# Performance work log

Measured on AMD Instinct MI355X. Metric: run time of the kernel, lower is better.

Reference implementation:

```python
import jax, jax.numpy as jnp
import numpy as np

D_MODEL = 768
NHEAD = 12
DK = D_MODEL // NHEAD
MAX_DIST = 1000.0
FF = 3072
POS_HIDDEN = 32  # hidden width of the relative-position bias MLP
EPS = 1e-5
B, L = 2, 1024


def setup_inputs() -> dict:
    key = jax.random.key(0)
    ks = jax.random.split(key, 24)

    def lin(k, i, o):  # torch-Linear-like init, stored as (in, out)
        return jax.random.uniform(k, (i, o), jnp.float32, -1.0, 1.0) / np.sqrt(i)

    return {
        "src": jax.random.normal(ks[0], (B, L, D_MODEL), jnp.float32),
        "src_x": jax.random.uniform(ks[1], (B, L), jnp.float32) * 1000.0,
        "src_y": jax.random.uniform(ks[2], (B, L), jnp.float32) * 1000.0,
        # attention projections (q,k,v,out)
        "Wq": lin(ks[3], D_MODEL, D_MODEL), "bq": jnp.zeros((D_MODEL,), jnp.float32),
        "Wk": lin(ks[4], D_MODEL, D_MODEL), "bk": jnp.zeros((D_MODEL,), jnp.float32),
        "Wv": lin(ks[5], D_MODEL, D_MODEL), "bv": jnp.zeros((D_MODEL,), jnp.float32),
        "Wo": lin(ks[6], D_MODEL, D_MODEL), "bo": jnp.zeros((D_MODEL,), jnp.float32),
        # relative-position bias MLP: 2 -> POS_HIDDEN -> NHEAD
        "P1": lin(ks[7], 2, POS_HIDDEN), "pb1": jnp.zeros((POS_HIDDEN,), jnp.float32),
        "P2": lin(ks[8], POS_HIDDEN, NHEAD), "pb2": jnp.zeros((NHEAD,), jnp.float32),
        # FFN
        "W1": lin(ks[9], D_MODEL, FF), "b1": jnp.zeros((FF,), jnp.float32),
        "W2": lin(ks[10], FF, D_MODEL), "b2": jnp.zeros((D_MODEL,), jnp.float32),
        # post-LN params
        "g1": jnp.ones((D_MODEL,), jnp.float32), "be1": jnp.zeros((D_MODEL,), jnp.float32),
        "g2": jnp.ones((D_MODEL,), jnp.float32), "be2": jnp.zeros((D_MODEL,), jnp.float32),
    }


def _layernorm(x, g, b):
    m = jnp.mean(x, axis=-1, keepdims=True)
    v = jnp.var(x, axis=-1, keepdims=True)
    return (x - m) * jax.lax.rsqrt(v + EPS) * g + b


def reference(src, src_x, src_y, Wq, bq, Wk, bk, Wv, bv, Wo, bo,
              P1, pb1, P2, pb2, W1, b1, W2, b2, g1, be1, g2, be2):
    b, l, _ = src.shape
    # projections -> (b, h, l, dk)
    q = (src @ Wq + bq).reshape(b, l, NHEAD, DK).transpose(0, 2, 1, 3)
    k = (src @ Wk + bk).reshape(b, l, NHEAD, DK).transpose(0, 2, 1, 3)
    v = (src @ Wv + bv).reshape(b, l, NHEAD, DK).transpose(0, 2, 1, 3)
    # 2D relative positions, clipped and normalized to [-1, 1]
    rx = jnp.clip(src_x[:, :, None] - src_x[:, None, :], -MAX_DIST, MAX_DIST) / MAX_DIST
    ry = jnp.clip(src_y[:, :, None] - src_y[:, None, :], -MAX_DIST, MAX_DIST) / MAX_DIST
    rel = jnp.stack([rx, ry], axis=-1)                        # (b, l, l, 2)
    bias = jax.nn.relu(rel @ P1 + pb1) @ P2 + pb2             # (b, l, l, h)
    bias = bias.transpose(0, 3, 1, 2)                         # (b, h, l, l)
    scores = jnp.einsum('bhqd,bhkd->bhqk', q, k) / np.sqrt(DK).astype(np.float32) + bias
    attn = jax.nn.softmax(scores, axis=-1)
    o = jnp.einsum('bhqk,bhkd->bhqd', attn, v).transpose(0, 2, 1, 3).reshape(b, l, D_MODEL)
    src2 = o @ Wo + bo
    x = _layernorm(src + src2, g1, be1)                       # post-LN residual 1
    ff = jax.nn.relu(x @ W1 + b1) @ W2 + b2                   # FFN
    return _layernorm(x + ff, g2, be2)                        # post-LN residual 2
```

## Files before the change

### kernel.cpp

```cpp
#include <hip/hip_runtime.h>
#include <math.h>

typedef unsigned short ushort_t;
typedef __attribute__((ext_vector_type(8))) short bf16x8;
typedef __attribute__((ext_vector_type(4))) float f32x4;

constexpr int kD      = 768;
constexpr int kNH     = 12;
constexpr int kDK     = 64;
constexpr int kFF     = 3072;
constexpr int kL      = 1024;
constexpr int kRows   = 2048;
constexpr float kEPS  = 1e-5f;

__device__ __forceinline__ ushort_t f2bf(float f) {
    union { float f; unsigned u; } v; v.f = f;
    unsigned r = (v.u + 0x7fffu + ((v.u >> 16) & 1u)) >> 16;
    return (ushort_t)r;
}
__device__ __forceinline__ float bf2f(ushort_t u) {
    union { unsigned u; float f; } v; v.u = ((unsigned)u) << 16; return v.f;
}

#define GL_LDS(gp, lp) __builtin_amdgcn_global_load_lds( \
    (const __attribute__((address_space(1))) void*)(gp), \
    (__attribute__((address_space(3))) void*)(lp), 16, 0, 0)

template<int RELU, int OUTBF, int ADDBIAS>
__device__ __forceinline__ void gemm_body(const ushort_t* __restrict__ A,
                                          const ushort_t* __restrict__ WT,
                                          const float* __restrict__ bias,
                                          void* __restrict__ Cout,
                                          int N, int K, int row0, int col0,
                                          int kbeg, int kend, ushort_t* lds)
{
    ushort_t* As = lds;
    ushort_t* Bs = lds + 4096;

    const int tid  = threadIdx.x;
    const int lane = tid & 63;
    const int wave = tid >> 6;
    const int wrow = (wave & 1) * 64;
    const int wcol = (wave >> 1) * 64;

    const int srow = wave * 16 + (lane >> 2);
    const int sk   = (lane & 3) * 8;
    const ushort_t* ga0 = A  + (size_t)(row0 + srow)      * K + sk;
    const ushort_t* ga1 = A  + (size_t)(row0 + srow + 64) * K + sk;
    const ushort_t* gb0 = WT + (size_t)(col0 + srow)      * K + sk;
    const ushort_t* gb1 = WT + (size_t)(col0 + srow + 64) * K + sk;
    ushort_t* la0 = As + wave * 512;
    ushort_t* la1 = As + 2048 + wave * 512;
    ushort_t* lb0 = Bs + wave * 512;
    ushort_t* lb1 = Bs + 2048 + wave * 512;

    const int fl = lane & 15, fq = lane >> 4;
    const ushort_t* fa[4];
    const ushort_t* fb[4];
    #pragma unroll
    for (int i = 0; i < 4; ++i) {
        fa[i] = As + (wrow + i * 16 + fl) * 32 + fq * 8;
        fb[i] = Bs + (wcol + i * 16 + fl) * 32 + fq * 8;
    }

    f32x4 acc[4][4] = {};

    for (int k0 = kbeg; k0 < kend; k0 += 32) {
        __syncthreads();
        GL_LDS(ga0 + k0, la0);
        GL_LDS(ga1 + k0, la1);
        GL_LDS(gb0 + k0, lb0);
        GL_LDS(gb1 + k0, lb1);
        __syncthreads();

        bf16x8 av[4], bv[4];
        #pragma unroll
        for (int i = 0; i < 4; ++i) {
            av[i] = *(const bf16x8*)fa[i];
            bv[i] = *(const bf16x8*)fb[i];
        }
        #pragma unroll
        for (int mi = 0; mi < 4; ++mi)
            #pragma unroll
            for (int ni = 0; ni < 4; ++ni)
                acc[mi][ni] = __builtin_amdgcn_mfma_f32_16x16x32_bf16(
                    av[mi], bv[ni], acc[mi][ni], 0, 0, 0);
    }

    #pragma unroll
    for (int mi = 0; mi < 4; ++mi) {
        const int m = wrow + mi * 16 + fq * 4;
        #pragma unroll
        for (int ni = 0; ni < 4; ++ni) {
            const int n = wcol + ni * 16 + fl;
            const float bb = ADDBIAS ? bias[col0 + n] : 0.f;
            #pragma unroll
            for (int r = 0; r < 4; ++r) {
                float v = acc[mi][ni][r] + bb;
                if (RELU) v = fmaxf(v, 0.f);
                const size_t idx = (size_t)(row0 + m + r) * N + col0 + n;
                if (OUTBF) ((ushort_t*)Cout)[idx] = f2bf(v);
                else       ((float*)Cout)[idx]    = v;
            }
        }
    }
}

template<int RELU, int OUTBF>
__global__ __launch_bounds__(256)
void gemm_kernel(const ushort_t* __restrict__ A, const ushort_t* __restrict__ WT,
                 const float* __restrict__ bias, void* __restrict__ Cout,
                 int N, int K)
{
    __shared__ ushort_t lds[8192];
    gemm_body<RELU, OUTBF, 1>(A, WT, bias, Cout, N, K,
                              blockIdx.y * 128, blockIdx.x * 128, 0, K, lds);
}

__global__ __launch_bounds__(256)
void gemm_splitk_kernel(const ushort_t* __restrict__ A, const ushort_t* __restrict__ WT,
                        float* __restrict__ parts, int N, int K, int kslice)
{
    __shared__ ushort_t lds[8192];
    const int z = blockIdx.z;
    float* out = parts + (size_t)z * kRows * N;
    gemm_body<0, 0, 0>(A, WT, nullptr, out, N, K,
                       blockIdx.y * 128, blockIdx.x * 128,
                       z * kslice, (z + 1) * kslice, lds);
}

__device__ __forceinline__ void wt_tile(const float* __restrict__ src,
                                        ushort_t* __restrict__ dst,
                                        int K, int N, int kt, int nt,
                                        float (*T)[65], int tid)
{
    #pragma unroll
    for (int i = 0; i < 4; ++i) {
        const int e = tid + i * 256;
        const int r = e >> 4;
        const int c = (e & 15) * 4;
        const float4 f = *(const float4*)&src[(size_t)(kt + r) * N + nt + c];
        T[c + 0][r] = f.x; T[c + 1][r] = f.y; T[c + 2][r] = f.z; T[c + 3][r] = f.w;
    }
    __syncthreads();
    #pragma unroll
    for (int i = 0; i < 4; ++i) {
        const int e = tid + i * 256;
        const int n = e >> 4;
        const int kc = (e & 15) * 4;
        ushort4 o;
        o.x = f2bf(T[n][kc + 0]); o.y = f2bf(T[n][kc + 1]);
        o.z = f2bf(T[n][kc + 2]); o.w = f2bf(T[n][kc + 3]);
        *(ushort4*)&dst[(size_t)(nt + n) * K + kt + kc] = o;
    }
}

__global__ __launch_bounds__(256)
void prep_kernel(const float* __restrict__ Wq, const float* __restrict__ Wk,
                 const float* __restrict__ Wv,
                 ushort_t* wqT, ushort_t* wkT, ushort_t* wvT,
                 const float* __restrict__ src, ushort_t* __restrict__ sb)
{
    __shared__ float T[64][65];
    const int bid = blockIdx.x;
    const int tid = threadIdx.x;

    if (bid < 432) {
        const int wz = bid / 144, t = bid - wz * 144;
        const float* s = (wz == 0) ? Wq : (wz == 1) ? Wk : Wv;
        ushort_t*   d = (wz == 0) ? wqT : (wz == 1) ? wkT : wvT;
        wt_tile(s, d, kD, kD, (t % 12) * 64, (t / 12) * 64, T, tid);
    } else {
        const int i = (bid - 432) * 256 + tid;
        const float4 f = ((const float4*)src)[i];
        ushort4 o;
        o.x = f2bf(f.x); o.y = f2bf(f.y); o.z = f2bf(f.z); o.w = f2bf(f.w);
        ((ushort4*)sb)[i] = o;
    }
}

struct BiasSmem {
    float P[32][16];
    float pb2l[12];
    float qxl[16], qyl[16], kxl[64], kyl[64];
    ushort_t Btile[12 * 1024];
};
struct AttnSmem {
    ushort_t Sp[4][16][72];
    ushort_t Ob[4][16][64];
    float    Ll[4][16];
};

__device__ __forceinline__ void bias_body(int bid, BiasSmem& S,
                 const float* __restrict__ sx, const float* __restrict__ sy,
                 const float* __restrict__ P1, const float* __restrict__ pb1,
                 const float* __restrict__ P2, const float* __restrict__ pb2,
                 ushort_t* __restrict__ biasb)
{
    const int b  = bid >> 10;
    const int qt = (bid >> 4) & 63;
    const int kt = bid & 15;
    const int tid = threadIdx.x;

    if (tid < 32) {
        S.P[tid][0] = P1[tid];
        S.P[tid][1] = P1[32 + tid];
        S.P[tid][2] = pb1[tid];
        S.P[tid][3] = 0.f;
    }
    for (int e = tid; e < 384; e += 256) S.P[e / 12][4 + e % 12] = P2[e];
    if (tid < 12) S.pb2l[tid] = pb2[tid];
    if (tid < 16) { S.qxl[tid] = sx[b * kL + qt * 16 + tid];
                    S.qyl[tid] = sy[b * kL + qt * 16 + tid]; }
    if (tid < 64) { S.kxl[tid] = sx[b * kL + kt * 64 + tid];
                    S.kyl[tid] = sy[b * kL + kt * 64 + tid]; }
    __syncthreads();

    const int ri = tid >> 4;
    const int fl = tid & 15;
    const int fq = ri >> 2, r = ri & 3;
    const int lane16 = fq * 16 + fl;
    const float xi = S.qxl[ri], yi = S.qyl[ri];

    float rx[4], ry[4];
    #pragma unroll
    for (int n = 0; n < 4; ++n) {
        const int cj = n * 16 + fl;
        rx[n] = fminf(fmaxf(xi - S.kxl[cj], -1000.f), 1000.f) * 1e-3f;
        ry[n] = fminf(fmaxf(yi - S.kyl[cj], -1000.f), 1000.f) * 1e-3f;
    }

    float acc[4][12] = {};
    #pragma unroll 4
    for (int u = 0; u < 32; ++u) {
        const float4 pc = *(const float4*)&S.P[u][0];
        const float4 w0 = *(const float4*)&S.P[u][4];
        const float4 w1 = *(const float4*)&S.P[u][8];
        const float4 w2 = *(const float4*)&S.P[u][12];
        float t[4];
        #pragma unroll
        for (int n = 0; n < 4; ++n)
            t[n] = fmaxf(fmaf(rx[n], pc.x, fmaf(ry[n], pc.y, pc.z)), 0.f);
        #pragma unroll
        for (int n = 0; n < 4; ++n) {
            acc[n][0]  = fmaf(t[n], w0.x, acc[n][0]);
            acc[n][1]  = fmaf(t[n], w0.y, acc[n][1]);
            acc[n][2]  = fmaf(t[n], w0.z, acc[n][2]);
            acc[n][3]  = fmaf(t[n], w0.w, acc[n][3]);
            acc[n][4]  = fmaf(t[n], w1.x, acc[n][4]);
            acc[n][5]  = fmaf(t[n], w1.y, acc[n][5]);
            acc[n][6]  = fmaf(t[n], w1.z, acc[n][6]);
            acc[n][7]  = fmaf(t[n], w1.w, acc[n][7]);
            acc[n][8]  = fmaf(t[n], w2.x, acc[n][8]);
            acc[n][9]  = fmaf(t[n], w2.y, acc[n][9]);
            acc[n][10] = fmaf(t[n], w2.z, acc[n][10]);
            acc[n][11] = fmaf(t[n], w2.w, acc[n][11]);
        }
    }

    #pragma unroll
    for (int h = 0; h < 12; ++h) {
        const float pb = S.pb2l[h] - 4.0f;
        #pragma unroll
        for (int n = 0; n < 4; ++n)
            S.Btile[h * 1024 + lane16 * 16 + n * 4 + r] = f2bf(acc[n][h] + pb);
    }
    __syncthreads();

    #pragma unroll
    for (int i = 0; i < 6; ++i) {
        const int off = (i * 256 + tid) * 8;
        const int h = off >> 10;
        const int inner = off & 1023;
        ushort_t* dst = biasb +
            (((size_t)(b * kNH + h) * 64 + qt) * 16 + kt) * 1024 + inner;
        *(uint4*)dst = *(const uint4*)&S.Btile[off];
    }
}

__global__ __launch_bounds__(256)
void qkv_bias_kernel(const ushort_t* __restrict__ A,
                     const ushort_t* wq, const ushort_t* wk, const ushort_t* wv,
                     const float* bq, const float* bk, const float* bv,
                     ushort_t* q, ushort_t* k, ushort_t* v,
                     const float* __restrict__ sx, const float* __restrict__ sy,
                     const float* __restrict__ P1, const float* __restrict__ pb1,
                     const float* __restrict__ P2, const float* __restrict__ pb2,
                     ushort_t* __restrict__ biasb)
{
    __shared__ __align__(16) char smem[sizeof(BiasSmem)];
    const int bid = blockIdx.x;

    if (bid < 288) {
        const int z = bid / 96, rem = bid - z * 96;
        const int bx = rem % 6, by = rem / 6;
        const ushort_t* WT; const float* bias; ushort_t* out;
        if (z == 0)      { WT = wq; bias = bq; out = q; }
        else if (z == 1) { WT = wk; bias = bk; out = k; }
        else             { WT = wv; bias = bv; out = v; }
        gemm_body<0, 1, 1>(A, WT, bias, out, kD, kD,
                           by * 128, bx * 128, 0, kD, (ushort_t*)smem);
    } else {
        bias_body(bid - 288, *(BiasSmem*)smem, sx, sy, P1, pb1, P2, pb2, biasb);
    }
}

__global__ __launch_bounds__(256)
void vtrans_kernel(const ushort_t* __restrict__ vb, ushort_t* __restrict__ vt)
{
    const int bh = blockIdx.x;
    const int b = bh / kNH, h = bh - b * kNH;
    const int j0 = blockIdx.y * 64;
    __shared__ ushort_t T[64][72];

    const int tid = threadIdx.x;
    {
        const int jr = tid & 63;
        const int c0 = (tid >> 6) * 16;
        const ushort_t* sp = vb + (size_t)(b * kL + j0 + jr) * kD + h * kDK + c0;
        uint4 u0 = *(const uint4*)sp;
        uint4 u1 = *(const uint4*)(sp + 8);
        const ushort_t* e0 = (const ushort_t*)&u0;
        const ushort_t* e1 = (const ushort_t*)&u1;
        #pragma unroll
        for (int jj = 0; jj < 8; ++jj) {
            T[c0 + jj][jr]     = e0[jj];
            T[c0 + 8 + jj][jr] = e1[jj];
        }
    }
    __syncthreads();
    {
        const int dr = tid >> 2;
        const int jc = (tid & 3) * 16;
        ushort_t* dp = vt + (size_t)(bh * 64 + dr) * kL + j0 + jc;
        *(uint4*)dp       = *(const uint4*)&T[dr][jc];
        *(uint4*)(dp + 8) = *(const uint4*)&T[dr][jc + 8];
    }
}

constexpr size_t kAttnWtSmem =
    sizeof(AttnSmem) > sizeof(float) * 64 * 65 ? sizeof(AttnSmem)
                                               : sizeof(float) * 64 * 65;

__global__ __launch_bounds__(256)
void attn_wt_kernel(const ushort_t* __restrict__ qg, const ushort_t* __restrict__ kg,
                    const ushort_t* __restrict__ vt, const ushort_t* __restrict__ biasb,
                    ushort_t* __restrict__ og,
                    const float* __restrict__ Wo, const float* __restrict__ W1,
                    const float* __restrict__ W2,
                    ushort_t* woT, ushort_t* w1T, ushort_t* w2T)
{
    __shared__ __align__(16) char smem[kAttnWtSmem];
    const int bid = blockIdx.x;
    const int tid = threadIdx.x;

    if (bid >= 1536) {
        float (*T)[65] = (float(*)[65])smem;
        const int t = bid - 1536;
        if (t < 144)      wt_tile(Wo, woT, kD,  kD,  (t % 12) * 64, (t / 12) * 64, T, tid);
        else if (t < 720) { const int t2 = t - 144;
                            wt_tile(W1, w1T, kD,  kFF, (t2 % 12) * 64, (t2 / 12) * 64, T, tid); }
        else              { const int t2 = t - 720;
                            wt_tile(W2, w2T, kFF, kD,  (t2 % 48) * 64, (t2 / 48) * 64, T, tid); }
        return;
    }

    AttnSmem& S = *(AttnSmem*)smem;
    const int bh = bid >> 6;
    const int qt = bid & 63;
    const int b  = bh / kNH, h = bh - b * kNH;
    const int q0 = qt * 16;
    const int z  = tid >> 6;
    const int lane = tid & 63;
    const int fl = lane & 15, fq = lane >> 4;

    const size_t qoff = (size_t)(b * kL + q0 + fl) * kD + h * kDK + fq * 8;
    const bf16x8 aq0 = *(const bf16x8*)(qg + qoff);
    const bf16x8 aq1 = *(const bf16x8*)(qg + qoff + 32);

    const ushort_t* kbase = kg + (size_t)(b * kL) * kD + h * kDK + fq * 8;
    const ushort_t* vbase = vt + (size_t)(bh * 64) * kL + fq * 8;
    const ushort_t* btile = biasb +
        ((size_t)(bh * 64 + qt) * 16 + z * 4) * 1024 + lane * 16;

    f32x4 accO[4] = {};
    float l_part[4] = {};

    bf16x8 kc[4][2];
    uint4 bc0, bc1;
    {
        const int k0 = z * 256;
        #pragma unroll
        for (int n = 0; n < 4; ++n) {
            const ushort_t* kr = kbase + (size_t)(k0 + n * 16 + fl) * kD;
            kc[n][0] = *(const bf16x8*)kr;
            kc[n][1] = *(const bf16x8*)(kr + 32);
        }
        bc0 = *(const uint4*)btile;
        bc1 = *(const uint4*)(btile + 8);
    }

    #pragma unroll
    for (int t = 0; t < 4; ++t) {
        const int k0 = z * 256 + t * 64;

        bf16x8 vv[4][2];
        #pragma unroll
        for (int n = 0; n < 4; ++n) {
            const ushort_t* vr = vbase + (size_t)(n * 16 + fl) * kL + k0;
            vv[n][0] = *(const bf16x8*)vr;
            vv[n][1] = *(const bf16x8*)(vr + 32);
        }

        f32x4 Sv[4] = {};
        #pragma unroll
        for (int n = 0; n < 4; ++n) {
            Sv[n] = __builtin_amdgcn_mfma_f32_16x16x32_bf16(aq0, kc[n][0], Sv[n], 0, 0, 0);
            Sv[n] = __builtin_amdgcn_mfma_f32_16x16x32_bf16(aq1, kc[n][1], Sv[n], 0, 0, 0);
        }

        bf16x8 kn[4][2];
        uint4 bn0, bn1;
        if (t < 3) {
            #pragma unroll
            for (int n = 0; n < 4; ++n) {
                const ushort_t* kr = kbase + (size_t)(k0 + 64 + n * 16 + fl) * kD;
                kn[n][0] = *(const bf16x8*)kr;
                kn[n][1] = *(const bf16x8*)(kr + 32);
            }
            bn0 = *(const uint4*)(btile + (t + 1) * 1024);
            bn1 = *(const uint4*)(btile + (t + 1) * 1024 + 8);
        }

        ushort_t bu[16];
        *(uint4*)&bu[0] = bc0;
        *(uint4*)&bu[8] = bc1;

        #pragma unroll
        for (int n = 0; n < 4; ++n)
            #pragma unroll
            for (int r = 0; r < 4; ++r) {
                const float e = __expf(fmaf(Sv[n][r], 0.125f, bf2f(bu[n * 4 + r])));
                Sv[n][r] = e;
                l_part[r] += e;
            }

        #pragma unroll
        for (int n = 0; n < 4; ++n)
            #pragma unroll
            for (int r = 0; r < 4; ++r)
                S.Sp[z][fq * 4 + r][n * 16 + fl] = f2bf(Sv[n][r]);

        const bf16x8 ap0 = *(const bf16x8*)&S.Sp[z][fl][fq * 8];
        const bf16x8 ap1 = *(const bf16x8*)&S.Sp[z][fl][32 + fq * 8];
        #pragma unroll
        for (int n = 0; n < 4; ++n) {
            accO[n] = __builtin_amdgcn_mfma_f32_16x16x32_bf16(ap0, vv[n][0], accO[n], 0, 0, 0);
            accO[n] = __builtin_amdgcn_mfma_f32_16x16x32_bf16(ap1, vv[n][1], accO[n], 0, 0, 0);
        }

        if (t < 3) {
            #pragma unroll
            for (int n = 0; n < 4; ++n) { kc[n][0] = kn[n][0]; kc[n][1] = kn[n][1]; }
            bc0 = bn0; bc1 = bn1;
        }
    }

    float l_full[4], inv[4];
    #pragma unroll
    for (int r = 0; r < 4; ++r) {
        float l = l_part[r];
        l += __shfl_xor(l, 1, 16);
        l += __shfl_xor(l, 2, 16);
        l += __shfl_xor(l, 4, 16);
        l += __shfl_xor(l, 8, 16);
        l_full[r] = l;
        inv[r] = 1.0f / l;
    }

    #pragma unroll
    for (int n = 0; n < 4; ++n)
        #pragma unroll
        for (int r = 0; r < 4; ++r)
            S.Ob[z][fq * 4 + r][n * 16 + fl] = f2bf(accO[n][r] * inv[r]);
    if (fl == 0) {
        #pragma unroll
        for (int r = 0; r < 4; ++r)
            S.Ll[z][fq * 4 + r] = l_full[r];
    }
    __syncthreads();

    {
        const int ri = tid >> 4;
        const int d0 = (tid & 15) * 4;
        const float w0 = S.Ll[0][ri], w1 = S.Ll[1][ri], w2 = S.Ll[2][ri], w3 = S.Ll[3][ri];
        const float winv = 1.0f / (w0 + w1 + w2 + w3);
        const float c0 = w0 * winv, c1 = w1 * winv, c2 = w2 * winv, c3 = w3 * winv;

        ushort_t o[4];
        #pragma unroll
        for (int j = 0; j < 4; ++j)
            o[j] = f2bf(fmaf(c0, bf2f(S.Ob[0][ri][d0 + j]),
                        fmaf(c1, bf2f(S.Ob[1][ri][d0 + j]),
                        fmaf(c2, bf2f(S.Ob[2][ri][d0 + j]),
                             c3 * bf2f(S.Ob[3][ri][d0 + j])))));
        *(uint2*)&og[(size_t)(b * kL + q0 + ri) * kD + h * kDK + d0] = *(const uint2*)o;
    }
}

template<int NPART, int DUAL>
__global__ __launch_bounds__(256)
void ln_kernel(const float* __restrict__ a, const float* __restrict__ parts,
               const float* __restrict__ bias,
               const float* __restrict__ g, const float* __restrict__ be,
               float* __restrict__ out, ushort_t* __restrict__ out_bf)
{
    const int row = blockIdx.x;
    const int tid = threadIdx.x;
    const float* pa = a + (size_t)row * kD;
    constexpr size_t NTOK = (size_t)kRows * kD;

    float v[3];
    float s = 0.f, sq = 0.f;
    #pragma unroll
    for (int i = 0; i < 3; ++i) {
        const int d = tid + i * 256;
        float t = pa[d] + bias[d];
        #pragma unroll
        for (int p = 0; p < NPART; ++p)
            t += parts[p * NTOK + (size_t)row * kD + d];
        v[i] = t;
        s  += t;
        sq += t * t;
    }
    #pragma unroll
    for (int off = 32; off > 0; off >>= 1) {
        s  += __shfl_down(s, off);
        sq += __shfl_down(sq, off);
    }
    __shared__ float bs[4], bq2[4];
    if ((tid & 63) == 0) { bs[tid >> 6] = s; bq2[tid >> 6] = sq; }
    __syncthreads();
    const float ts = bs[0] + bs[1] + bs[2] + bs[3];
    const float tq = bq2[0] + bq2[1] + bq2[2] + bq2[3];
    const float invn = 1.0f / (float)kD;
    const float mean = ts * invn;
    const float var  = tq * invn - mean * mean;
    const float rstd = rsqrtf(var + kEPS);

    float* po = out + (size_t)row * kD;
    #pragma unroll
    for (int i = 0; i < 3; ++i) {
        const int d = tid + i * 256;
        const float o = (v[i] - mean) * rstd * g[d] + be[d];
        po[d] = o;
        if (DUAL) out_bf[(size_t)row * kD + d] = f2bf(o);
    }
}

extern "C" void kernel_launch(void* const* d_in, const int* in_sizes, int n_in,
                              void* d_out, int out_size, void* d_ws, size_t ws_size,
                              hipStream_t stream)
{
    const float* src = (const float*)d_in[0];
    const float* sx  = (const float*)d_in[1];
    const float* sy  = (const float*)d_in[2];
    const float* Wq  = (const float*)d_in[3];  const float* bq  = (const float*)d_in[4];
    const float* Wk  = (const float*)d_in[5];  const float* bk  = (const float*)d_in[6];
    const float* Wv  = (const float*)d_in[7];  const float* bv  = (const float*)d_in[8];
    const float* Wo  = (const float*)d_in[9];  const float* bo  = (const float*)d_in[10];
    const float* P1  = (const float*)d_in[11]; const float* pb1 = (const float*)d_in[12];
    const float* P2  = (const float*)d_in[13]; const float* pb2 = (const float*)d_in[14];
    const float* W1  = (const float*)d_in[15]; const float* b1  = (const float*)d_in[16];
    const float* W2  = (const float*)d_in[17]; const float* b2  = (const float*)d_in[18];
    const float* g1  = (const float*)d_in[19]; const float* be1 = (const float*)d_in[20];
    const float* g2  = (const float*)d_in[21]; const float* be2 = (const float*)d_in[22];

    constexpr size_t W768  = 768u * 768u;
    constexpr size_t W3072 = 768u * 3072u;
    constexpr size_t NTOK  = (size_t)kRows * kD;

    ushort_t* wsu = (ushort_t*)d_ws;
    ushort_t* wqT = wsu;
    ushort_t* wkT = wqT + W768;
    ushort_t* wvT = wkT + W768;
    ushort_t* qb  = wvT + W768;
    ushort_t* kb  = qb + NTOK;
    ushort_t* vb  = kb + NTOK;
    ushort_t* sb  = vb + NTOK;
    ushort_t* vtb = sb + NTOK;
    ushort_t* biasb = vtb + NTOK;
    ushort_t* woT   = biasb;
    ushort_t* w1T   = woT + W768;
    ushort_t* w2T   = w1T + W3072;
    float*    xb    = (float*)(w2T + W3072);
    ushort_t* h1bf  = (ushort_t*)(xb + NTOK);
    float*    s2p   = (float*)h1bf;
    float*    ff2p  = (float*)(h1bf + 4 * NTOK);
    ushort_t* xbf   = qb;

    const dim3 blk(256);

    prep_kernel<<<dim3(1968), blk, 0, stream>>>(Wq, Wk, Wv, wqT, wkT, wvT, src, sb);

    qkv_bias_kernel<<<dim3(2336), blk, 0, stream>>>(
        sb, wqT, wkT, wvT, bq, bk, bv, qb, kb, vb,
        sx, sy, P1, pb1, P2, pb2, biasb);

    vtrans_kernel<<<dim3(2 * kNH, kL / 64), blk, 0, stream>>>(vb, vtb);

    attn_wt_kernel<<<dim3(2832), blk, 0, stream>>>(
        qb, kb, vtb, biasb, sb, Wo, W1, W2,
        (ushort_t*)(ff2p + 3 * NTOK),
        (ushort_t*)(ff2p + 3 * NTOK) + W768,
        (ushort_t*)(ff2p + 3 * NTOK) + W768 + W3072);

    ushort_t* woT2 = (ushort_t*)(ff2p + 3 * NTOK);
    ushort_t* w1T2 = woT2 + W768;
    ushort_t* w2T2 = w1T2 + W3072;

    gemm_splitk_kernel<<<dim3(kD / 128, kRows / 128, 2), blk, 0, stream>>>(
        sb, woT2, s2p, kD, kD, kD / 2);

    ln_kernel<2, 1><<<dim3(kRows), blk, 0, stream>>>(src, s2p, bo, g1, be1, xb, xbf);

    gemm_kernel<1, 1><<<dim3(kFF / 128, kRows / 128), blk, 0, stream>>>(
        xbf, w1T2, b1, h1bf, kFF, kD);

    gemm_splitk_kernel<<<dim3(kD / 128, kRows / 128, 3), blk, 0, stream>>>(
        h1bf, w2T2, ff2p, kD, kFF, kFF / 3);

    ln_kernel<3, 0><<<dim3(kRows), blk, 0, stream>>>(xb, ff2p, b2, g2, be2,
                                                     (float*)d_out, nullptr);
}
```

Baseline: 290.9 us.

## Give each attention wave its own query tile over full key range, drop cross-wave merge

Each wave in an attention block now handles a separate 16-row query tile across all 1024 keys, instead of four waves splitting the key range of one tile. This removes the LDS reduction, the __syncthreads and the weighted merge of partial outputs, and cuts the attention block count by a factor of four. A swizzled block index spreads heads and query tiles across XCDs. In exchange each wave runs a longer serial loop, and there are fewer blocks available to hide latency.

```diff
diff --git a/kernel.cpp b/kernel.cpp
--- a/kernel.cpp
+++ b/kernel.cpp
@@ -187,8 +187,6 @@
 };
 struct AttnSmem {
     ushort_t Sp[4][16][72];
-    ushort_t Ob[4][16][64];
-    float    Ll[4][16];
 };
 
 __device__ __forceinline__ void bias_body(int bid, BiasSmem& S,
@@ -354,9 +352,9 @@
     const int bid = blockIdx.x;
     const int tid = threadIdx.x;
 
-    if (bid >= 1536) {
+    if (bid >= 384) {
         float (*T)[65] = (float(*)[65])smem;
-        const int t = bid - 1536;
+        const int t = bid - 384;
         if (t < 144)      wt_tile(Wo, woT, kD,  kD,  (t % 12) * 64, (t / 12) * 64, T, tid);
         else if (t < 720) { const int t2 = t - 144;
                             wt_tile(W1, w1T, kD,  kFF, (t2 % 12) * 64, (t2 / 12) * 64, T, tid); }
@@ -366,13 +364,15 @@
     }
 
     AttnSmem& S = *(AttnSmem*)smem;
-    const int bh = bid >> 6;
-    const int qt = bid & 63;
+    const int swz  = (bid & 7) * 48 + (bid >> 3);
+    const int bh   = swz >> 4;
+    const int qt64 = swz & 15;
     const int b  = bh / kNH, h = bh - b * kNH;
-    const int q0 = qt * 16;
     const int z  = tid >> 6;
     const int lane = tid & 63;
     const int fl = lane & 15, fq = lane >> 4;
+    const int qt = qt64 * 4 + z;
+    const int q0 = qt * 16;
 
     const size_t qoff = (size_t)(b * kL + q0 + fl) * kD + h * kDK + fq * 8;
     const bf16x8 aq0 = *(const bf16x8*)(qg + qoff);
@@ -381,7 +381,7 @@
     const ushort_t* kbase = kg + (size_t)(b * kL) * kD + h * kDK + fq * 8;
     const ushort_t* vbase = vt + (size_t)(bh * 64) * kL + fq * 8;
     const ushort_t* btile = biasb +
-        ((size_t)(bh * 64 + qt) * 16 + z * 4) * 1024 + lane * 16;
+        ((size_t)(bh * 64 + qt) * 16) * 1024 + lane * 16;
 
     f32x4 accO[4] = {};
     float l_part[4] = {};
@@ -389,10 +389,9 @@
     bf16x8 kc[4][2];
     uint4 bc0, bc1;
     {
-        const int k0 = z * 256;
         #pragma unroll
         for (int n = 0; n < 4; ++n) {
-            const ushort_t* kr = kbase + (size_t)(k0 + n * 16 + fl) * kD;
+            const ushort_t* kr = kbase + (size_t)(n * 16 + fl) * kD;
             kc[n][0] = *(const bf16x8*)kr;
             kc[n][1] = *(const bf16x8*)(kr + 32);
         }
@@ -400,9 +399,9 @@
         bc1 = *(const uint4*)(btile + 8);
     }
 
-    #pragma unroll
-    for (int t = 0; t < 4; ++t) {
-        const int k0 = z * 256 + t * 64;
+    #pragma unroll 4
+    for (int t = 0; t < 16; ++t) {
+        const int k0 = t * 64;
 
         bf16x8 vv[4][2];
         #pragma unroll
@@ -421,7 +420,7 @@
 
         bf16x8 kn[4][2];
         uint4 bn0, bn1;
-        if (t < 3) {
+        if (t < 15) {
             #pragma unroll
             for (int n = 0; n < 4; ++n) {
                 const ushort_t* kr = kbase + (size_t)(k0 + 64 + n * 16 + fl) * kD;
@@ -459,14 +458,14 @@
             accO[n] = __builtin_amdgcn_mfma_f32_16x16x32_bf16(ap1, vv[n][1], accO[n], 0, 0, 0);
         }
 
-        if (t < 3) {
+        if (t < 15) {
             #pragma unroll
             for (int n = 0; n < 4; ++n) { kc[n][0] = kn[n][0]; kc[n][1] = kn[n][1]; }
             bc0 = bn0; bc1 = bn1;
         }
     }
 
-    float l_full[4], inv[4];
+    float inv[4];
     #pragma unroll
     for (int r = 0; r < 4; ++r) {
         float l = l_part[r];
@@ -474,7 +473,6 @@
         l += __shfl_xor(l, 2, 16);
         l += __shfl_xor(l, 4, 16);
         l += __shfl_xor(l, 8, 16);
-        l_full[r] = l;
         inv[r] = 1.0f / l;
     }
 
@@ -482,29 +480,12 @@
     for (int n = 0; n < 4; ++n)
         #pragma unroll
         for (int r = 0; r < 4; ++r)
-            S.Ob[z][fq * 4 + r][n * 16 + fl] = f2bf(accO[n][r] * inv[r]);
-    if (fl == 0) {
-        #pragma unroll
-        for (int r = 0; r < 4; ++r)
-            S.Ll[z][fq * 4 + r] = l_full[r];
-    }
-    __syncthreads();
+            S.Sp[z][fq * 4 + r][n * 16 + fl] = f2bf(accO[n][r] * inv[r]);
 
     {
-        const int ri = tid >> 4;
-        const int d0 = (tid & 15) * 4;
-        const float w0 = S.Ll[0][ri], w1 = S.Ll[1][ri], w2 = S.Ll[2][ri], w3 = S.Ll[3][ri];
-        const float winv = 1.0f / (w0 + w1 + w2 + w3);
-        const float c0 = w0 * winv, c1 = w1 * winv, c2 = w2 * winv, c3 = w3 * winv;
-
-        ushort_t o[4];
-        #pragma unroll
-        for (int j = 0; j < 4; ++j)
-            o[j] = f2bf(fmaf(c0, bf2f(S.Ob[0][ri][d0 + j]),
-                        fmaf(c1, bf2f(S.Ob[1][ri][d0 + j]),
-                        fmaf(c2, bf2f(S.Ob[2][ri][d0 + j]),
-                             c3 * bf2f(S.Ob[3][ri][d0 + j])))));
-        *(uint2*)&og[(size_t)(b * kL + q0 + ri) * kD + h * kDK + d0] = *(const uint2*)o;
+        ushort_t* dp = og + (size_t)(b * kL + q0 + fl) * kD + h * kDK + fq * 16;
+        *(uint4*)dp       = *(const uint4*)&S.Sp[z][fl][fq * 16];
+        *(uint4*)(dp + 8) = *(const uint4*)&S.Sp[z][fl][fq * 16 + 8];
     }
 }
 
@@ -609,7 +590,7 @@
 
     vtrans_kernel<<<dim3(2 * kNH, kL / 64), blk, 0, stream>>>(vb, vtb);
 
-    attn_wt_kernel<<<dim3(2832), blk, 0, stream>>>(
+    attn_wt_kernel<<<dim3(1680), blk, 0, stream>>>(
         qb, kb, vtb, biasb, sb, Wo, W1, W2,
         (ushort_t*)(ff2p + 3 * NTOK),
         (ushort_t*)(ff2p + 3 * NTOK) + W768,
```

After: 300.0 us. 3.1% more time.

## Process two query tiles per attention block with two-way key split and swizzled block order

Applied to the files above, without the earlier changes.

Each attention block now covers 32 query rows: two waves per 16-row query tile, each wave handling half the keys (512) rather than a quarter. This halves the number of attention blocks and the split-softmax merge width, and a swizzle spreads consecutive block IDs across heads. The intent is to cut per-block overhead and partial-merge work and to improve K/V cache locality. The cost is a longer serial loop per wave with less parallelism for latency hiding.

```diff
diff --git a/kernel.cpp b/kernel.cpp
--- a/kernel.cpp
+++ b/kernel.cpp
@@ -354,9 +354,9 @@
     const int bid = blockIdx.x;
     const int tid = threadIdx.x;
 
-    if (bid >= 1536) {
+    if (bid >= 768) {
         float (*T)[65] = (float(*)[65])smem;
-        const int t = bid - 1536;
+        const int t = bid - 768;
         if (t < 144)      wt_tile(Wo, woT, kD,  kD,  (t % 12) * 64, (t / 12) * 64, T, tid);
         else if (t < 720) { const int t2 = t - 144;
                             wt_tile(W1, w1T, kD,  kFF, (t2 % 12) * 64, (t2 / 12) * 64, T, tid); }
@@ -366,13 +366,18 @@
     }
 
     AttnSmem& S = *(AttnSmem*)smem;
-    const int bh = bid >> 6;
-    const int qt = bid & 63;
+    const int swz  = (bid & 7) * 96 + (bid >> 3);
+    const int bh   = swz >> 5;
+    const int qt32 = swz & 31;
     const int b  = bh / kNH, h = bh - b * kNH;
-    const int q0 = qt * 16;
     const int z  = tid >> 6;
+    const int qs = z & 1;
+    const int kh = z >> 1;
     const int lane = tid & 63;
     const int fl = lane & 15, fq = lane >> 4;
+    const int qt = qt32 * 2 + qs;
+    const int q0 = qt * 16;
+    const int kbeg = kh * 512;
 
     const size_t qoff = (size_t)(b * kL + q0 + fl) * kD + h * kDK + fq * 8;
     const bf16x8 aq0 = *(const bf16x8*)(qg + qoff);
@@ -381,7 +386,7 @@
     const ushort_t* kbase = kg + (size_t)(b * kL) * kD + h * kDK + fq * 8;
     const ushort_t* vbase = vt + (size_t)(bh * 64) * kL + fq * 8;
     const ushort_t* btile = biasb +
-        ((size_t)(bh * 64 + qt) * 16 + z * 4) * 1024 + lane * 16;
+        ((size_t)(bh * 64 + qt) * 16 + kh * 8) * 1024 + lane * 16;
 
     f32x4 accO[4] = {};
     float l_part[4] = {};
@@ -389,10 +394,9 @@
     bf16x8 kc[4][2];
     uint4 bc0, bc1;
     {
-        const int k0 = z * 256;
         #pragma unroll
         for (int n = 0; n < 4; ++n) {
-            const ushort_t* kr = kbase + (size_t)(k0 + n * 16 + fl) * kD;
+            const ushort_t* kr = kbase + (size_t)(kbeg + n * 16 + fl) * kD;
             kc[n][0] = *(const bf16x8*)kr;
             kc[n][1] = *(const bf16x8*)(kr + 32);
         }
@@ -400,9 +404,9 @@
         bc1 = *(const uint4*)(btile + 8);
     }
 
-    #pragma unroll
-    for (int t = 0; t < 4; ++t) {
-        const int k0 = z * 256 + t * 64;
+    #pragma unroll 4
+    for (int t = 0; t < 8; ++t) {
+        const int k0 = kbeg + t * 64;
 
         bf16x8 vv[4][2];
         #pragma unroll
@@ -421,7 +425,7 @@
 
         bf16x8 kn[4][2];
         uint4 bn0, bn1;
-        if (t < 3) {
+        if (t < 7) {
             #pragma unroll
             for (int n = 0; n < 4; ++n) {
                 const ushort_t* kr = kbase + (size_t)(k0 + 64 + n * 16 + fl) * kD;
@@ -459,7 +463,7 @@
             accO[n] = __builtin_amdgcn_mfma_f32_16x16x32_bf16(ap1, vv[n][1], accO[n], 0, 0, 0);
         }
 
-        if (t < 3) {
+        if (t < 7) {
             #pragma unroll
             for (int n = 0; n < 4; ++n) { kc[n][0] = kn[n][0]; kc[n][1] = kn[n][1]; }
             bc0 = bn0; bc1 = bn1;
@@ -491,20 +495,21 @@
     __syncthreads();
 
     {
-        const int ri = tid >> 4;
-        const int d0 = (tid & 15) * 4;
-        const float w0 = S.Ll[0][ri], w1 = S.Ll[1][ri], w2 = S.Ll[2][ri], w3 = S.Ll[3][ri];
-        const float winv = 1.0f / (w0 + w1 + w2 + w3);
-        const float c0 = w0 * winv, c1 = w1 * winv, c2 = w2 * winv, c3 = w3 * winv;
-
-        ushort_t o[4];
-        #pragma unroll
-        for (int j = 0; j < 4; ++j)
-            o[j] = f2bf(fmaf(c0, bf2f(S.Ob[0][ri][d0 + j]),
-                        fmaf(c1, bf2f(S.Ob[1][ri][d0 + j]),
-                        fmaf(c2, bf2f(S.Ob[2][ri][d0 + j]),
-                             c3 * bf2f(S.Ob[3][ri][d0 + j])))));
-        *(uint2*)&og[(size_t)(b * kL + q0 + ri) * kD + h * kDK + d0] = *(const uint2*)o;
+        const int ri = tid >> 3;
+        const int d0 = (tid & 7) * 8;
+        const int qs2 = ri >> 4, rr = ri & 15;
+        const int z0 = qs2, z1 = 2 + qs2;
+        const float w0 = S.Ll[z0][rr], w1 = S.Ll[z1][rr];
+        const float winv = 1.0f / (w0 + w1);
+        const float c0 = w0 * winv, c1 = w1 * winv;
+
+        ushort_t o[8];
+        #pragma unroll
+        for (int j = 0; j < 8; ++j)
+            o[j] = f2bf(fmaf(c0, bf2f(S.Ob[z0][rr][d0 + j]),
+                             c1 * bf2f(S.Ob[z1][rr][d0 + j])));
+        ushort_t* dp = og + (size_t)(b * kL + qt32 * 32 + ri) * kD + h * kDK + d0;
+        *(uint4*)dp = *(const uint4*)o;
     }
 }
 
@@ -609,7 +614,7 @@
 
     vtrans_kernel<<<dim3(2 * kNH, kL / 64), blk, 0, stream>>>(vb, vtb);
 
-    attn_wt_kernel<<<dim3(2832), blk, 0, stream>>>(
+    attn_wt_kernel<<<dim3(2064), blk, 0, stream>>>(
         qb, kb, vtb, biasb, sb, Wo, W1, W2,
         (ushort_t*)(ff2p + 3 * NTOK),
         (ushort_t*)(ff2p + 3 * NTOK) + W768,
```

New measurement: 288.7 us. Within noise of the previous version (-0.7%).
